# Performance work log

Hardware: AMD Instinct MI355X
Metric: run time of the kernel (lower is better)

The kernel has to match this reference:

```python
import jax, jax.numpy as jnp
import numpy as np

B, S, H = 2, 1024, 2048
E, K, I = 32, 4, 512   # num_experts, top_k, moe_intermediate
IS = 512               # shared_expert_intermediate


def setup_inputs() -> dict:
    key = jax.random.key(0)
    ks = jax.random.split(key, 10)
    s = 0.02
    return {
        "hidden_states": jax.random.normal(ks[0], (B, S, H), jnp.float32),
        "Wr": jax.random.normal(ks[1], (E, H), jnp.float32) * s,      # router gate
        "Wg": jax.random.normal(ks[2], (E, I, H), jnp.float32) * s,   # expert gate_proj
        "Wu": jax.random.normal(ks[3], (E, I, H), jnp.float32) * s,   # expert up_proj
        "Wd": jax.random.normal(ks[4], (E, H, I), jnp.float32) * s,   # expert down_proj
        "Wsg": jax.random.normal(ks[5], (IS, H), jnp.float32) * s,    # shared gate_proj
        "Wsu": jax.random.normal(ks[6], (IS, H), jnp.float32) * s,    # shared up_proj
        "Wsd": jax.random.normal(ks[7], (H, IS), jnp.float32) * s,    # shared down_proj
        "Wsgate": jax.random.normal(ks[8], (1, H), jnp.float32) * s,  # shared_expert_gate
    }


def reference(hidden_states, Wr, Wg, Wu, Wd, Wsg, Wsu, Wsd, Wsgate):
    b, s, h = hidden_states.shape
    x = hidden_states.reshape(-1, h)                      # [T, H]
    T = x.shape[0]

    # router: softmax in fp32, top-k, renormalize (norm_topk_prob=True)
    router_logits = x @ Wr.T                               # [T, E]
    rw = jax.nn.softmax(router_logits.astype(jnp.float32), axis=-1)
    vals, idx = jax.lax.top_k(rw, K)                       # [T, K]
    vals = vals / jnp.sum(vals, axis=-1, keepdims=True)
    vals = vals.astype(x.dtype)

    # combine-weight matrix: zeros except selected experts
    C = jnp.zeros((T, E), x.dtype).at[jnp.arange(T)[:, None], idx].add(vals)

    # all experts evaluate all tokens (calibrate_all_experts path); combine zeros non-selected
    g = jnp.einsum('th,eih->tei', x, Wg)                   # [T, E, I]
    u = jnp.einsum('th,eih->tei', x, Wu)
    hact = jax.nn.silu(g) * u
    moe_out = jnp.einsum('tei,ehi,te->th', hact, Wd, C)    # weighted combine

    # shared expert with sigmoid gate
    shared = (jax.nn.silu(x @ Wsg.T) * (x @ Wsu.T)) @ Wsd.T
    gate = jax.nn.sigmoid(x @ Wsgate.T)                    # [T, 1]
    out = (moe_out + gate * shared).reshape(b, s, h)
    return out, router_logits
```

## Files before the change

### kernel.cpp

```cpp
#include <hip/hip_runtime.h>
#include <math.h>

#define T_N 2048
#define H_N 2048
#define E_N 32
#define I_N 512
#define NA_MOE (T_N*4)
#define NA_ALL (NA_MOE + T_N)
#define BM 256
#define BK 32
#define MAXT 72

typedef short s16x8 __attribute__((ext_vector_type(8)));
typedef float f32x4 __attribute__((ext_vector_type(4)));

__device__ inline short f2bf(float f){
    unsigned int u = __float_as_uint(f);
    u = (u + 0x7fffu + ((u >> 16) & 1u)) >> 16;
    return (short)u;
}

__device__ inline s16x8 cvt8(float4 f0, float4 f1){
    s16x8 v;
    v[0]=f2bf(f0.x); v[1]=f2bf(f0.y); v[2]=f2bf(f0.z); v[3]=f2bf(f0.w);
    v[4]=f2bf(f1.x); v[5]=f2bf(f1.y); v[6]=f2bf(f1.z); v[7]=f2bf(f1.w);
    return v;
}

__global__ __launch_bounds__(256) void cast_x_kernel(const float* __restrict__ x,
                                                     short* __restrict__ xbf){
    size_t i = (size_t)(blockIdx.x * 256 + threadIdx.x) * 8;
    float4 a = *(const float4*)(x + i);
    float4 b = *(const float4*)(x + i + 4);
    *(s16x8*)(xbf + i) = cvt8(a, b);
}

__global__ __launch_bounds__(64) void router_kernel(
    const float* __restrict__ x, const float* __restrict__ Wr,
    const float* __restrict__ Wsgate,
    float* __restrict__ logits_out, int* __restrict__ tidx, float* __restrict__ tw,
    int* __restrict__ perm, float* __restrict__ wgt, int* __restrict__ counts)
{
    const int t = blockIdx.x, lane = threadIdx.x;
    const float* xr = x + (size_t)t * H_N;
    float xv[32];
    #pragma unroll
    for (int i = 0; i < 32; i++) xv[i] = xr[i*64 + lane];
    __shared__ float lg[34];
    for (int e = 0; e < 33; e++){
        const float* wr = (e < 32) ? (Wr + (size_t)e * H_N) : Wsgate;
        double s = 0.0;
        #pragma unroll
        for (int i = 0; i < 32; i++) s += (double)xv[i] * (double)wr[i*64 + lane];
        #pragma unroll
        for (int o = 32; o > 0; o >>= 1) s += __shfl_down(s, o);
        if (lane == 0) lg[e] = (float)s;
    }
    __syncthreads();
    if (lane < 32) logits_out[(size_t)t*32 + lane] = lg[lane];
    if (lane == 0){
        float m = lg[0];
        for (int e = 1; e < 32; e++) m = fmaxf(m, lg[e]);
        unsigned mask = 0; int sel[4]; float sv[4]; float s4 = 0.f;
        for (int k = 0; k < 4; k++){
            int best = -1; float bv = -1e30f;
            for (int e = 0; e < 32; e++)
                if (!((mask >> e) & 1u) && lg[e] > bv){ bv = lg[e]; best = e; }
            mask |= 1u << best; sel[k] = best;
            float p = expf(lg[best] - m); sv[k] = p; s4 += p;
        }
        for (int k = 0; k < 4; k++){
            tidx[t*4 + k] = sel[k];
            tw[t*4 + k]   = sv[k] / s4;
            atomicAdd(&counts[sel[k]], 1);
        }
        perm[NA_MOE + t] = t;
        wgt[NA_MOE + t]  = 1.f / (1.f + expf(-lg[32]));
    }
}

__global__ void scan_kernel(int* ctrl){
    if (threadIdx.x == 0){
        int* counts = ctrl; int* eoff = ctrl + 128; int* ecnt = ctrl + 192;
        int acc = 0;
        for (int e = 0; e < 32; e++){ eoff[e] = acc; ecnt[e] = counts[e]; acc += counts[e]; }
        eoff[32] = NA_MOE; ecnt[32] = T_N;
        int nt = 0;
        for (int e = 0; e < 33; e++){
            int c = ecnt[e];
            for (int m = 0; m * BM < c; m++) ctrl[260 + nt++] = (e << 16) | m;
        }
        ctrl[256] = nt;
    }
    if (threadIdx.x < 64) ctrl[64 + threadIdx.x] = 0;
}

__global__ __launch_bounds__(256) void scatter_kernel(
    const int* __restrict__ tidx, const float* __restrict__ tw,
    int* __restrict__ perm, float* __restrict__ wgt, int* ctrl)
{
    int t = blockIdx.x * 256 + threadIdx.x;
    if (t >= T_N) return;
    const int* eoff = ctrl + 128; int* cursor = ctrl + 64;
    for (int k = 0; k < 4; k++){
        int e = tidx[t*4 + k];
        int pos = eoff[e] + atomicAdd(&cursor[e], 1);
        perm[pos] = t; wgt[pos] = tw[t*4 + k];
    }
}

__global__ __launch_bounds__(512) void gemm1_kernel(
    const short* __restrict__ xbf,
    const float* __restrict__ Wg, const float* __restrict__ Wu,
    const float* __restrict__ Wsg, const float* __restrict__ Wsu,
    const int* __restrict__ perm, const int* __restrict__ ctrl,
    short* __restrict__ hact)
{
    const int tile = blockIdx.x >> 3;
    if (tile >= ctrl[256]) return;
    const int wrk = ctrl[260 + tile];
    const int e   = wrk >> 16;
    const int m0  = (wrk & 0xffff) << 8;
    const int cnt = ctrl[192 + e];
    const int off = ctrl[128 + e];
    const int n0  = (blockIdx.x & 7) << 6;

    __shared__ s16x8 lsA[4*256];
    __shared__ s16x8 lsBg[4*64];
    __shared__ s16x8 lsBu[4*64];

    const int tid = threadIdx.x;
    const int r_a = tid & 255;
    const int kca = tid >> 8;
    const short* arow = nullptr;
    if (m0 + r_a < cnt) arow = xbf + (size_t)perm[off + m0 + r_a] * H_N;

    const int cb  = tid & 255;
    const int kcb = cb & 3, rb = cb >> 2;
    const float* brow;
    if (e < 32){
        const float* Wbase = (tid < 256) ? Wg : Wu;
        brow = Wbase + ((size_t)e * I_N + (n0 + rb)) * H_N + kcb*8;
    } else {
        const float* Wbase = (tid < 256) ? Wsg : Wsu;
        brow = Wbase + (size_t)(n0 + rb) * H_N + kcb*8;
    }
    s16x8* lsBmine = (tid < 256) ? lsBg : lsBu;

    const int wid = tid >> 6, lane = tid & 63;
    const int wm = wid >> 1, wn = wid & 1;
    const int kg = lane >> 4, l15 = lane & 15;

    f32x4 accg[4][2], accu[4][2];
    #pragma unroll
    for (int a = 0; a < 4; a++)
        #pragma unroll
        for (int b = 0; b < 2; b++)
            #pragma unroll
            for (int j = 0; j < 4; j++){ accg[a][b][j] = 0.f; accu[a][b][j] = 0.f; }

    s16x8 a0{}, a1{};
    float4 f0, f1;
    if (arow){
        a0 = *(const s16x8*)(arow + kca*8);
        a1 = *(const s16x8*)(arow + (kca+2)*8);
    }
    f0 = *(const float4*)(brow);
    f1 = *(const float4*)(brow + 4);

    for (int k0 = 0; k0 < H_N; k0 += BK){
        __syncthreads();
        lsA[kca*256 + r_a]     = a0;
        lsA[(kca+2)*256 + r_a] = a1;
        lsBmine[kcb*64 + rb]   = cvt8(f0, f1);
        __syncthreads();
        if (k0 + BK < H_N){
            if (arow){
                a0 = *(const s16x8*)(arow + k0 + BK + kca*8);
                a1 = *(const s16x8*)(arow + k0 + BK + (kca+2)*8);
            }
            f0 = *(const float4*)(brow + k0 + BK);
            f1 = *(const float4*)(brow + k0 + BK + 4);
        }
        s16x8 bg[2], bu[2];
        #pragma unroll
        for (int nf = 0; nf < 2; nf++){
            bg[nf] = lsBg[kg*64 + wn*32 + nf*16 + l15];
            bu[nf] = lsBu[kg*64 + wn*32 + nf*16 + l15];
        }
        #pragma unroll
        for (int mf = 0; mf < 4; mf++){
            s16x8 a = lsA[kg*256 + wm*64 + mf*16 + l15];
            #pragma unroll
            for (int nf = 0; nf < 2; nf++){
                accg[mf][nf] = __builtin_amdgcn_mfma_f32_16x16x32_bf16(a, bg[nf], accg[mf][nf], 0, 0, 0);
                accu[mf][nf] = __builtin_amdgcn_mfma_f32_16x16x32_bf16(a, bu[nf], accu[mf][nf], 0, 0, 0);
            }
        }
    }
    #pragma unroll
    for (int mf = 0; mf < 4; mf++){
        #pragma unroll
        for (int j = 0; j < 4; j++){
            int row = m0 + wm*64 + mf*16 + kg*4 + j;
            if (row < cnt){
                #pragma unroll
                for (int nf = 0; nf < 2; nf++){
                    int col = n0 + wn*32 + nf*16 + l15;
                    float g = accg[mf][nf][j], u = accu[mf][nf][j];
                    float h = g / (1.f + expf(-g)) * u;
                    hact[(size_t)(off + row) * I_N + col] = f2bf(h);
                }
            }
        }
    }
}

__global__ __launch_bounds__(512) void gemm2_kernel(
    const short* __restrict__ hact,
    const float* __restrict__ Wd, const float* __restrict__ Wsd,
    const int* __restrict__ perm, const float* __restrict__ wgt,
    const int* __restrict__ ctrl, float* __restrict__ out)
{
    const int tile = blockIdx.x >> 5;
    if (tile >= ctrl[256]) return;
    const int wrk = ctrl[260 + tile];
    const int e   = wrk >> 16;
    const int m0  = (wrk & 0xffff) << 8;
    const int cnt = ctrl[192 + e];
    const int off = ctrl[128 + e];
    const int n0  = (blockIdx.x & 31) << 6;

    __shared__ s16x8 lsA[4*256];
    __shared__ s16x8 lsB[4*64];

    const int tid = threadIdx.x;
    const int r_a = tid & 255;
    const int kca = tid >> 8;
    const short* arow = nullptr;
    if (m0 + r_a < cnt) arow = hact + (size_t)(off + m0 + r_a) * I_N;

    const int cb  = tid & 255;
    const int kcb = cb & 3, rb = cb >> 2;
    const float* brow = (e < 32) ? (Wd  + ((size_t)e * H_N + (n0 + rb)) * I_N + kcb*8)
                                 : (Wsd + (size_t)(n0 + rb) * I_N + kcb*8);

    const int wid = tid >> 6, lane = tid & 63;
    const int wm = wid >> 1, wn = wid & 1;
    const int kg = lane >> 4, l15 = lane & 15;

    f32x4 acc[4][2];
    #pragma unroll
    for (int a = 0; a < 4; a++)
        #pragma unroll
        for (int b = 0; b < 2; b++)
            #pragma unroll
            for (int j = 0; j < 4; j++) acc[a][b][j] = 0.f;

    s16x8 a0{}, a1{};
    float4 f0, f1;
    if (arow){
        a0 = *(const s16x8*)(arow + kca*8);
        a1 = *(const s16x8*)(arow + (kca+2)*8);
    }
    if (tid < 256){
        f0 = *(const float4*)(brow);
        f1 = *(const float4*)(brow + 4);
    }

    for (int k0 = 0; k0 < I_N; k0 += BK){
        __syncthreads();
        lsA[kca*256 + r_a]     = a0;
        lsA[(kca+2)*256 + r_a] = a1;
        if (tid < 256) lsB[kcb*64 + rb] = cvt8(f0, f1);
        __syncthreads();
        if (k0 + BK < I_N){
            if (arow){
                a0 = *(const s16x8*)(arow + k0 + BK + kca*8);
                a1 = *(const s16x8*)(arow + k0 + BK + (kca+2)*8);
            }
            if (tid < 256){
                f0 = *(const float4*)(brow + k0 + BK);
                f1 = *(const float4*)(brow + k0 + BK + 4);
            }
        }
        s16x8 b[2];
        #pragma unroll
        for (int nf = 0; nf < 2; nf++)
            b[nf] = lsB[kg*64 + wn*32 + nf*16 + l15];
        #pragma unroll
        for (int mf = 0; mf < 4; mf++){
            s16x8 a = lsA[kg*256 + wm*64 + mf*16 + l15];
            #pragma unroll
            for (int nf = 0; nf < 2; nf++)
                acc[mf][nf] = __builtin_amdgcn_mfma_f32_16x16x32_bf16(a, b[nf], acc[mf][nf], 0, 0, 0);
        }
    }
    #pragma unroll
    for (int mf = 0; mf < 4; mf++){
        #pragma unroll
        for (int j = 0; j < 4; j++){
            int row = m0 + wm*64 + mf*16 + kg*4 + j;
            if (row < cnt){
                int aidx = off + row;
                int tok  = perm[aidx];
                float w  = wgt[aidx];
                #pragma unroll
                for (int nf = 0; nf < 2; nf++){
                    int col = n0 + wn*32 + nf*16 + l15;
                    atomicAdd(&out[(size_t)tok * H_N + col], w * acc[mf][nf][j]);
                }
            }
        }
    }
}

extern "C" void kernel_launch(void* const* d_in, const int* in_sizes, int n_in,
                              void* d_out, int out_size, void* d_ws, size_t ws_size,
                              hipStream_t stream)
{
    const float* x      = (const float*)d_in[0];
    const float* Wr     = (const float*)d_in[1];
    const float* Wg     = (const float*)d_in[2];
    const float* Wu     = (const float*)d_in[3];
    const float* Wd     = (const float*)d_in[4];
    const float* Wsg    = (const float*)d_in[5];
    const float* Wsu    = (const float*)d_in[6];
    const float* Wsd    = (const float*)d_in[7];
    const float* Wsgate = (const float*)d_in[8];

    float* out    = (float*)d_out;
    float* logits = out + (size_t)T_N * H_N;

    char* ws = (char*)d_ws;
    short* xbf  = (short*)ws;
    short* hact = (short*)(ws + 8388608);
    int*   perm = (int*)(ws + 18874368);
    float* wgt  = (float*)(ws + 18915328);
    int*   tidx = (int*)(ws + 18956288);
    float* tw   = (float*)(ws + 18989056);
    int*   ctrl = (int*)(ws + 19021824);

    hipMemsetAsync(d_out, 0, (size_t)T_N * H_N * sizeof(float), stream);
    hipMemsetAsync(ctrl, 0, 256 * sizeof(int), stream);

    cast_x_kernel<<<2048, 256, 0, stream>>>(x, xbf);
    router_kernel<<<T_N, 64, 0, stream>>>(x, Wr, Wsgate, logits, tidx, tw, perm, wgt, ctrl);
    scan_kernel<<<1, 64, 0, stream>>>(ctrl);
    scatter_kernel<<<T_N/256, 256, 0, stream>>>(tidx, tw, perm, wgt, ctrl);
    gemm1_kernel<<<MAXT*8,  512, 0, stream>>>(xbf, Wg, Wu, Wsg, Wsu, perm, ctrl, hact);
    gemm2_kernel<<<MAXT*32, 512, 0, stream>>>(hact, Wd, Wsd, perm, wgt, ctrl, out);
}
```

Before: 450.2 us.

## Halve GEMM M-tile to 128 and replace atomic scatter with bf16 buffer plus combine

Shrinks the M tile from 256 to 128 rows with 256-thread blocks in both expert GEMMs, raising the max tile count, to cut padding waste on small per-expert groups and improve occupancy. When enough workspace exists, gemm2 writes per-assignment outputs as bf16 into a staging buffer, and a new combine kernel sums each token's top-k plus shared contributions. This replaces the fp32 atomicAdd scatter and the output memset. It adds a roughly 40 MB write and read of intermediate data and an extra bf16 rounding of expert outputs before combining.

```diff
diff --git a/kernel.cpp b/kernel.cpp
--- a/kernel.cpp
+++ b/kernel.cpp
@@ -7,9 +7,9 @@
 #define I_N 512
 #define NA_MOE (T_N*4)
 #define NA_ALL (NA_MOE + T_N)
-#define BM 256
+#define BM 128
 #define BK 32
-#define MAXT 72
+#define MAXT 112
 
 typedef short s16x8 __attribute__((ext_vector_type(8)));
 typedef float f32x4 __attribute__((ext_vector_type(4)));
@@ -19,7 +19,9 @@
     u = (u + 0x7fffu + ((u >> 16) & 1u)) >> 16;
     return (short)u;
 }
-
+__device__ inline float bf2f(short s){
+    return __uint_as_float(((unsigned int)(unsigned short)s) << 16);
+}
 __device__ inline s16x8 cvt8(float4 f0, float4 f1){
     s16x8 v;
     v[0]=f2bf(f0.x); v[1]=f2bf(f0.y); v[2]=f2bf(f0.z); v[3]=f2bf(f0.w);
@@ -97,7 +99,8 @@
 
 __global__ __launch_bounds__(256) void scatter_kernel(
     const int* __restrict__ tidx, const float* __restrict__ tw,
-    int* __restrict__ perm, float* __restrict__ wgt, int* ctrl)
+    int* __restrict__ perm, float* __restrict__ wgt, int* __restrict__ apos,
+    int* ctrl)
 {
     int t = blockIdx.x * 256 + threadIdx.x;
     if (t >= T_N) return;
@@ -105,11 +108,11 @@
     for (int k = 0; k < 4; k++){
         int e = tidx[t*4 + k];
         int pos = eoff[e] + atomicAdd(&cursor[e], 1);
-        perm[pos] = t; wgt[pos] = tw[t*4 + k];
-    }
-}
-
-__global__ __launch_bounds__(512) void gemm1_kernel(
+        perm[pos] = t; wgt[pos] = tw[t*4 + k]; apos[t*4 + k] = pos;
+    }
+}
+
+__global__ __launch_bounds__(256, 3) void gemm1_kernel(
     const short* __restrict__ xbf,
     const float* __restrict__ Wg, const float* __restrict__ Wu,
     const float* __restrict__ Wsg, const float* __restrict__ Wsu,
@@ -120,32 +123,30 @@
     if (tile >= ctrl[256]) return;
     const int wrk = ctrl[260 + tile];
     const int e   = wrk >> 16;
-    const int m0  = (wrk & 0xffff) << 8;
+    const int m0  = (wrk & 0xffff) << 7;
     const int cnt = ctrl[192 + e];
     const int off = ctrl[128 + e];
     const int n0  = (blockIdx.x & 7) << 6;
 
-    __shared__ s16x8 lsA[4*256];
+    __shared__ s16x8 lsA[4*128];
     __shared__ s16x8 lsBg[4*64];
     __shared__ s16x8 lsBu[4*64];
 
     const int tid = threadIdx.x;
-    const int r_a = tid & 255;
-    const int kca = tid >> 8;
+    const int r_a = tid & 127;
+    const int kca = tid >> 7;
     const short* arow = nullptr;
     if (m0 + r_a < cnt) arow = xbf + (size_t)perm[off + m0 + r_a] * H_N;
 
-    const int cb  = tid & 255;
-    const int kcb = cb & 3, rb = cb >> 2;
-    const float* brow;
+    const int rb = tid >> 2, kcb = tid & 3;
+    const float *browg, *browu;
     if (e < 32){
-        const float* Wbase = (tid < 256) ? Wg : Wu;
-        brow = Wbase + ((size_t)e * I_N + (n0 + rb)) * H_N + kcb*8;
+        browg = Wg + ((size_t)e * I_N + (n0 + rb)) * H_N + kcb*8;
+        browu = Wu + ((size_t)e * I_N + (n0 + rb)) * H_N + kcb*8;
     } else {
-        const float* Wbase = (tid < 256) ? Wsg : Wsu;
-        brow = Wbase + (size_t)(n0 + rb) * H_N + kcb*8;
-    }
-    s16x8* lsBmine = (tid < 256) ? lsBg : lsBu;
+        browg = Wsg + (size_t)(n0 + rb) * H_N + kcb*8;
+        browu = Wsu + (size_t)(n0 + rb) * H_N + kcb*8;
+    }
 
     const int wid = tid >> 6, lane = tid & 63;
     const int wm = wid >> 1, wn = wid & 1;
@@ -160,41 +161,41 @@
             for (int j = 0; j < 4; j++){ accg[a][b][j] = 0.f; accu[a][b][j] = 0.f; }
 
     s16x8 a0{}, a1{};
-    float4 f0, f1;
     if (arow){
         a0 = *(const s16x8*)(arow + kca*8);
         a1 = *(const s16x8*)(arow + (kca+2)*8);
     }
-    f0 = *(const float4*)(brow);
-    f1 = *(const float4*)(brow + 4);
+    float4 g0 = *(const float4*)(browg);
+    float4 g1 = *(const float4*)(browg + 4);
+    float4 u0 = *(const float4*)(browu);
+    float4 u1 = *(const float4*)(browu + 4);
 
     for (int k0 = 0; k0 < H_N; k0 += BK){
         __syncthreads();
-        lsA[kca*256 + r_a]     = a0;
-        lsA[(kca+2)*256 + r_a] = a1;
-        lsBmine[kcb*64 + rb]   = cvt8(f0, f1);
+        lsA[kca*128 + r_a]     = a0;
+        lsA[(kca+2)*128 + r_a] = a1;
+        lsBg[kcb*64 + rb]      = cvt8(g0, g1);
+        lsBu[kcb*64 + rb]      = cvt8(u0, u1);
         __syncthreads();
         if (k0 + BK < H_N){
             if (arow){
                 a0 = *(const s16x8*)(arow + k0 + BK + kca*8);
                 a1 = *(const s16x8*)(arow + k0 + BK + (kca+2)*8);
             }
-            f0 = *(const float4*)(brow + k0 + BK);
-            f1 = *(const float4*)(brow + k0 + BK + 4);
-        }
-        s16x8 bg[2], bu[2];
-        #pragma unroll
-        for (int nf = 0; nf < 2; nf++){
-            bg[nf] = lsBg[kg*64 + wn*32 + nf*16 + l15];
-            bu[nf] = lsBu[kg*64 + wn*32 + nf*16 + l15];
+            g0 = *(const float4*)(browg + k0 + BK);
+            g1 = *(const float4*)(browg + k0 + BK + 4);
+            u0 = *(const float4*)(browu + k0 + BK);
+            u1 = *(const float4*)(browu + k0 + BK + 4);
         }
         #pragma unroll
         for (int mf = 0; mf < 4; mf++){
-            s16x8 a = lsA[kg*256 + wm*64 + mf*16 + l15];
+            s16x8 a = lsA[kg*128 + wm*64 + mf*16 + l15];
             #pragma unroll
             for (int nf = 0; nf < 2; nf++){
-                accg[mf][nf] = __builtin_amdgcn_mfma_f32_16x16x32_bf16(a, bg[nf], accg[mf][nf], 0, 0, 0);
-                accu[mf][nf] = __builtin_amdgcn_mfma_f32_16x16x32_bf16(a, bu[nf], accu[mf][nf], 0, 0, 0);
+                s16x8 bg = lsBg[kg*64 + wn*32 + nf*16 + l15];
+                s16x8 bu = lsBu[kg*64 + wn*32 + nf*16 + l15];
+                accg[mf][nf] = __builtin_amdgcn_mfma_f32_16x16x32_bf16(a, bg, accg[mf][nf], 0, 0, 0);
+                accu[mf][nf] = __builtin_amdgcn_mfma_f32_16x16x32_bf16(a, bu, accu[mf][nf], 0, 0, 0);
             }
         }
     }
@@ -216,32 +217,32 @@
     }
 }
 
-__global__ __launch_bounds__(512) void gemm2_kernel(
+template<int USE_Y>
+__global__ __launch_bounds__(256) void gemm2_kernel(
     const short* __restrict__ hact,
     const float* __restrict__ Wd, const float* __restrict__ Wsd,
     const int* __restrict__ perm, const float* __restrict__ wgt,
-    const int* __restrict__ ctrl, float* __restrict__ out)
+    const int* __restrict__ ctrl, float* __restrict__ out, short* __restrict__ y)
 {
     const int tile = blockIdx.x >> 5;
     if (tile >= ctrl[256]) return;
     const int wrk = ctrl[260 + tile];
     const int e   = wrk >> 16;
-    const int m0  = (wrk & 0xffff) << 8;
+    const int m0  = (wrk & 0xffff) << 7;
     const int cnt = ctrl[192 + e];
     const int off = ctrl[128 + e];
     const int n0  = (blockIdx.x & 31) << 6;
 
-    __shared__ s16x8 lsA[4*256];
+    __shared__ s16x8 lsA[4*128];
     __shared__ s16x8 lsB[4*64];
 
     const int tid = threadIdx.x;
-    const int r_a = tid & 255;
-    const int kca = tid >> 8;
+    const int r_a = tid & 127;
+    const int kca = tid >> 7;
     const short* arow = nullptr;
     if (m0 + r_a < cnt) arow = hact + (size_t)(off + m0 + r_a) * I_N;
 
-    const int cb  = tid & 255;
-    const int kcb = cb & 3, rb = cb >> 2;
+    const int rb = tid >> 2, kcb = tid & 3;
     const float* brow = (e < 32) ? (Wd  + ((size_t)e * H_N + (n0 + rb)) * I_N + kcb*8)
                                  : (Wsd + (size_t)(n0 + rb) * I_N + kcb*8);
 
@@ -258,42 +259,35 @@
             for (int j = 0; j < 4; j++) acc[a][b][j] = 0.f;
 
     s16x8 a0{}, a1{};
-    float4 f0, f1;
     if (arow){
         a0 = *(const s16x8*)(arow + kca*8);
         a1 = *(const s16x8*)(arow + (kca+2)*8);
     }
-    if (tid < 256){
-        f0 = *(const float4*)(brow);
-        f1 = *(const float4*)(brow + 4);
-    }
+    float4 f0 = *(const float4*)(brow);
+    float4 f1 = *(const float4*)(brow + 4);
 
     for (int k0 = 0; k0 < I_N; k0 += BK){
         __syncthreads();
-        lsA[kca*256 + r_a]     = a0;
-        lsA[(kca+2)*256 + r_a] = a1;
-        if (tid < 256) lsB[kcb*64 + rb] = cvt8(f0, f1);
+        lsA[kca*128 + r_a]     = a0;
+        lsA[(kca+2)*128 + r_a] = a1;
+        lsB[kcb*64 + rb]       = cvt8(f0, f1);
         __syncthreads();
         if (k0 + BK < I_N){
             if (arow){
                 a0 = *(const s16x8*)(arow + k0 + BK + kca*8);
                 a1 = *(const s16x8*)(arow + k0 + BK + (kca+2)*8);
             }
-            if (tid < 256){
-                f0 = *(const float4*)(brow + k0 + BK);
-                f1 = *(const float4*)(brow + k0 + BK + 4);
-            }
-        }
-        s16x8 b[2];
-        #pragma unroll
-        for (int nf = 0; nf < 2; nf++)
-            b[nf] = lsB[kg*64 + wn*32 + nf*16 + l15];
+            f0 = *(const float4*)(brow + k0 + BK);
+            f1 = *(const float4*)(brow + k0 + BK + 4);
+        }
         #pragma unroll
         for (int mf = 0; mf < 4; mf++){
-            s16x8 a = lsA[kg*256 + wm*64 + mf*16 + l15];
+            s16x8 a = lsA[kg*128 + wm*64 + mf*16 + l15];
             #pragma unroll
-            for (int nf = 0; nf < 2; nf++)
-                acc[mf][nf] = __builtin_amdgcn_mfma_f32_16x16x32_bf16(a, b[nf], acc[mf][nf], 0, 0, 0);
+            for (int nf = 0; nf < 2; nf++){
+                s16x8 b = lsB[kg*64 + wn*32 + nf*16 + l15];
+                acc[mf][nf] = __builtin_amdgcn_mfma_f32_16x16x32_bf16(a, b, acc[mf][nf], 0, 0, 0);
+            }
         }
     }
     #pragma unroll
@@ -303,16 +297,52 @@
             int row = m0 + wm*64 + mf*16 + kg*4 + j;
             if (row < cnt){
                 int aidx = off + row;
-                int tok  = perm[aidx];
-                float w  = wgt[aidx];
-                #pragma unroll
-                for (int nf = 0; nf < 2; nf++){
-                    int col = n0 + wn*32 + nf*16 + l15;
-                    atomicAdd(&out[(size_t)tok * H_N + col], w * acc[mf][nf][j]);
+                if (USE_Y){
+                    #pragma unroll
+                    for (int nf = 0; nf < 2; nf++){
+                        int col = n0 + wn*32 + nf*16 + l15;
+                        y[(size_t)aidx * H_N + col] = f2bf(acc[mf][nf][j]);
+                    }
+                } else {
+                    int tok = perm[aidx];
+                    float w = wgt[aidx];
+                    #pragma unroll
+                    for (int nf = 0; nf < 2; nf++){
+                        int col = n0 + wn*32 + nf*16 + l15;
+                        atomicAdd(&out[(size_t)tok * H_N + col], w * acc[mf][nf][j]);
+                    }
                 }
             }
         }
     }
+}
+
+__global__ __launch_bounds__(256) void combine_kernel(
+    const short* __restrict__ y, const int* __restrict__ apos,
+    const float* __restrict__ tw, const float* __restrict__ wgt,
+    float* __restrict__ out)
+{
+    const int t = blockIdx.x;
+    const int c0 = threadIdx.x * 8;
+    float acc[8];
+    {
+        float ws = wgt[NA_MOE + t];
+        s16x8 v = *(const s16x8*)(y + (size_t)(NA_MOE + t) * H_N + c0);
+        #pragma unroll
+        for (int j = 0; j < 8; j++) acc[j] = ws * bf2f(v[j]);
+    }
+    #pragma unroll
+    for (int k = 0; k < 4; k++){
+        int p   = apos[t*4 + k];
+        float w = tw[t*4 + k];
+        s16x8 v = *(const s16x8*)(y + (size_t)p * H_N + c0);
+        #pragma unroll
+        for (int j = 0; j < 8; j++) acc[j] += w * bf2f(v[j]);
+    }
+    float4 o0 = make_float4(acc[0], acc[1], acc[2], acc[3]);
+    float4 o1 = make_float4(acc[4], acc[5], acc[6], acc[7]);
+    *(float4*)(out + (size_t)t * H_N + c0)     = o0;
+    *(float4*)(out + (size_t)t * H_N + c0 + 4) = o1;
 }
 
 extern "C" void kernel_launch(void* const* d_in, const int* in_sizes, int n_in,
@@ -339,15 +369,25 @@
     float* wgt  = (float*)(ws + 18915328);
     int*   tidx = (int*)(ws + 18956288);
     float* tw   = (float*)(ws + 18989056);
-    int*   ctrl = (int*)(ws + 19021824);
-
-    hipMemsetAsync(d_out, 0, (size_t)T_N * H_N * sizeof(float), stream);
+    int*   apos = (int*)(ws + 19021824);
+    int*   ctrl = (int*)(ws + 19054592);
+    short* y    = (short*)(ws + 19056640);
+    const size_t Y_END = 19056640ull + 41943040ull;
+    const bool use_y = (ws_size >= Y_END);
+
     hipMemsetAsync(ctrl, 0, 256 * sizeof(int), stream);
+    if (!use_y)
+        hipMemsetAsync(d_out, 0, (size_t)T_N * H_N * sizeof(float), stream);
 
     cast_x_kernel<<<2048, 256, 0, stream>>>(x, xbf);
     router_kernel<<<T_N, 64, 0, stream>>>(x, Wr, Wsgate, logits, tidx, tw, perm, wgt, ctrl);
     scan_kernel<<<1, 64, 0, stream>>>(ctrl);
-    scatter_kernel<<<T_N/256, 256, 0, stream>>>(tidx, tw, perm, wgt, ctrl);
-    gemm1_kernel<<<MAXT*8,  512, 0, stream>>>(xbf, Wg, Wu, Wsg, Wsu, perm, ctrl, hact);
-    gemm2_kernel<<<MAXT*32, 512, 0, stream>>>(hact, Wd, Wsd, perm, wgt, ctrl, out);
-}
+    scatter_kernel<<<T_N/256, 256, 0, stream>>>(tidx, tw, perm, wgt, apos, ctrl);
+    gemm1_kernel<<<MAXT*8, 256, 0, stream>>>(xbf, Wg, Wu, Wsg, Wsu, perm, ctrl, hact);
+    if (use_y){
+        gemm2_kernel<1><<<MAXT*32, 256, 0, stream>>>(hact, Wd, Wsd, perm, wgt, ctrl, out, y);
+        combine_kernel<<<T_N, 256, 0, stream>>>(y, apos, tw, wgt, out);
+    } else {
+        gemm2_kernel<0><<<MAXT*32, 256, 0, stream>>>(hact, Wd, Wsd, perm, wgt, ctrl, out, y);
+    }
+}
```

After: 363.8 us. 1.24x faster.
